# Kernel tuning notes

Hardware: AMD Instinct MI355X
Metric: run time of the kernel (lower is better)

The kernel has to match this reference:

```python
import jax, jax.numpy as jnp
from jax import lax
import numpy as np

GRID = 256   # spatial_shape of the sparse voxel volume (D=H=W)
N_ACTIVE = 500000
K = 5        # kernel_size=5, padding=2, stride=1 -> 'same' box-sum conv


def setup_inputs() -> dict:
    key = jax.random.key(0)
    k1, k2 = jax.random.split(key)
    feats = jax.random.normal(k1, (N_ACTIVE,), dtype=jnp.float32)
    coords = jax.random.randint(k2, (N_ACTIVE, 3), 0, GRID, dtype=jnp.int32)
    return {"feats": feats, "coords": coords}


def reference(feats, coords):
    # Densify the sparse tensor: scatter active-voxel features into [B=1, C=1, D, H, W].
    vol = jnp.zeros((1, 1, GRID, GRID, GRID), dtype=feats.dtype)
    vol = vol.at[0, 0, coords[:, 0], coords[:, 1], coords[:, 2]].add(feats)
    # Frozen all-ones 5x5x5 kernel (weight.data = ones, requires_grad=False), no bias.
    kernel = jnp.ones((1, 1, K, K, K), dtype=feats.dtype)  # OIDHW
    pad = K // 2
    out = lax.conv_general_dilated(
        vol, kernel,
        window_strides=(1, 1, 1),
        padding=[(pad, pad)] * 3,
        dimension_numbers=("NCDHW", "OIDHW", "NCDHW"),
    )
    # Original returns a list of one dense volume; return the array.
    return out
```

## Files before the change

kernel.cpp:

```cpp
#include <hip/hip_runtime.h>
#include <hip/hip_fp16.h>

#define GRIDN 256
#define NVOX (GRIDN * GRIDN * GRIDN)
#define NYT  32
#define NBKT (GRIDN * NYT)
#define NSUB 8
#define SBCAP 32

#define TYF   8
#define WROWS 12
#define ZS    8
#define NTHR  256

typedef float floatx4 __attribute__((ext_vector_type(4)));

#define BAR_LDS()                                              \
    do {                                                       \
        asm volatile("s_waitcnt lgkmcnt(0)" ::: "memory");     \
        __builtin_amdgcn_sched_barrier(0);                     \
        __builtin_amdgcn_s_barrier();                          \
        __builtin_amdgcn_sched_barrier(0);                     \
    } while (0)

__global__ __launch_bounds__(NTHR) void k_bin(const float* __restrict__ feats,
                                              const int* __restrict__ coords,
                                              int* __restrict__ cnt,
                                              unsigned int* __restrict__ rec, int n) {
    int i = blockIdx.x * NTHR + threadIdx.x;
    if (i >= n) return;
    int d = coords[3 * i + 0];
    int h = coords[3 * i + 1];
    int w = coords[3 * i + 2];
    int s   = blockIdx.x & (NSUB - 1);
    int key = s * NBKT + d * NYT + (h >> 3);
    int slot = atomicAdd(&cnt[key], 1);
    if (slot < SBCAP) {
        unsigned int r = (unsigned int)w | ((unsigned int)h << 8)
                       | ((unsigned int)__half_as_ushort(__float2half(feats[i])) << 16);
        rec[((size_t)key << 5) + slot] = r;
    }
}

__global__ __launch_bounds__(NTHR) void k_fused_sparse(const int* __restrict__ cnt,
                                                       const unsigned int* __restrict__ rec,
                                                       float* __restrict__ out) {
    __shared__ float Xp[3][WROWS][256];
    __shared__ int   cms[ZS + 4][24];
    __shared__ int   rbs[ZS + 4][24];

    const int tid = threadIdx.x;
    int wg  = blockIdx.x;
    int swz = (wg & 7) * 128 + (wg >> 3);
    const int y0 = (swz & 31) * TYF;
    const int z0 = (swz >> 5) * ZS;

    const int xq  = (tid & 63) * 4;
    const int yy2 = (tid >> 6) * 2;
    const int yt0 = y0 >> 3;

    for (int idx = tid; idx < (ZS + 4) * 24; idx += NTHR) {
        int k = idx / 24, q = idx - 24 * k;
        int t = q >> 3, s = q & 7;
        int zi = z0 - 2 + k;
        int yt = yt0 - 1 + t;
        int m = 0, b = 0;
        if ((unsigned)zi < (unsigned)GRIDN && (unsigned)yt < (unsigned)NYT) {
            int key = s * NBKT + zi * NYT + yt;
            m = min(cnt[key], SBCAP);
            b = key << 5;
        }
        cms[k][q] = m;
        rbs[k][q] = b;
    }
    for (int idx = tid; idx < 3 * WROWS * 64; idx += NTHR)
        ((float4*)Xp)[idx] = make_float4(0.f, 0.f, 0.f, 0.f);
    BAR_LDS();

    const int q0s = (0 * 256 + tid) >> 5, sl0 = tid & 31;
    const int q1s = (1 * 256 + tid) >> 5, sl1 = tid & 31;
    const int q2s = (2 * 256 + tid) >> 5, sl2 = tid & 31;

    auto fetch = [&](int k, unsigned int& r0, unsigned int& r1, unsigned int& r2) {
        r0 = (sl0 < cms[k][q0s]) ? rec[rbs[k][q0s] + sl0] : 0u;
        r1 = (sl1 < cms[k][q1s]) ? rec[rbs[k][q1s] + sl1] : 0u;
        r2 = (sl2 < cms[k][q2s]) ? rec[rbs[k][q2s] + sl2] : 0u;
    };

    unsigned int p0, p1, p2;
    fetch(0, p0, p1, p2);

    float4 a0 = {0,0,0,0}, a1 = {0,0,0,0}, a2 = {0,0,0,0}, a3 = {0,0,0,0}, a4 = {0,0,0,0};
    float4 b0 = {0,0,0,0}, b1 = {0,0,0,0}, b2 = {0,0,0,0}, b3 = {0,0,0,0}, b4 = {0,0,0,0};

    for (int k = 0; k <= ZS + 4; ++k) {
        unsigned int n0 = 0, n1 = 0, n2 = 0;
        if (k + 1 <= ZS + 3) fetch(k + 1, n0, n1, n2);

        if (k <= ZS + 3) {
            float (*buf)[256] = Xp[k % 3];
            auto scat = [&](unsigned int r, int ok) {
                if (!ok) return;
                int x  = r & 255;
                int y  = (r >> 8) & 255;
                int ry = y - y0 + 2;
                if ((unsigned)ry < (unsigned)WROWS) {
                    float f = __half2float(__ushort_as_half((unsigned short)(r >> 16)));
                    #pragma unroll
                    for (int dx = -2; dx <= 2; ++dx) {
                        int cc = x + dx;
                        if ((unsigned)cc < 256u)
                            atomicAdd(&buf[ry][cc], f);
                    }
                }
            };
            scat(p0, sl0 < cms[k][q0s]);
            scat(p1, sl1 < cms[k][q1s]);
            scat(p2, sl2 < cms[k][q2s]);
        }
        if (k + 1 <= ZS + 3) {
            float4* zb = (float4*)Xp[(k + 1) % 3];
            for (int idx = tid; idx < WROWS * 64; idx += NTHR)
                zb[idx] = make_float4(0.f, 0.f, 0.f, 0.f);
        }
        if (k >= 1) {
            float (*pb)[256] = Xp[(k - 1) % 3];
            float4 r0 = *(const float4*)&pb[yy2 + 0][xq];
            float4 r1 = *(const float4*)&pb[yy2 + 1][xq];
            float4 r2 = *(const float4*)&pb[yy2 + 2][xq];
            float4 r3 = *(const float4*)&pb[yy2 + 3][xq];
            float4 r4 = *(const float4*)&pb[yy2 + 4][xq];
            float4 r5 = *(const float4*)&pb[yy2 + 5][xq];
            float4 sm, v0, v1;
            sm.x = r1.x + r2.x + r3.x + r4.x;  sm.y = r1.y + r2.y + r3.y + r4.y;
            sm.z = r1.z + r2.z + r3.z + r4.z;  sm.w = r1.w + r2.w + r3.w + r4.w;
            v0.x = sm.x + r0.x; v0.y = sm.y + r0.y; v0.z = sm.z + r0.z; v0.w = sm.w + r0.w;
            v1.x = sm.x + r5.x; v1.y = sm.y + r5.y; v1.z = sm.z + r5.z; v1.w = sm.w + r5.w;
            a0 = a1; a1 = a2; a2 = a3; a3 = a4; a4 = v0;
            b0 = b1; b1 = b2; b2 = b3; b3 = b4; b4 = v1;
            int j = k - 1;
            if (j >= 4) {
                int zo = z0 + j - 4;
                floatx4 s0, s1;
                s0.x = a0.x + a1.x + a2.x + a3.x + a4.x;
                s0.y = a0.y + a1.y + a2.y + a3.y + a4.y;
                s0.z = a0.z + a1.z + a2.z + a3.z + a4.z;
                s0.w = a0.w + a1.w + a2.w + a3.w + a4.w;
                s1.x = b0.x + b1.x + b2.x + b3.x + b4.x;
                s1.y = b0.y + b1.y + b2.y + b3.y + b4.y;
                s1.z = b0.z + b1.z + b2.z + b3.z + b4.z;
                s1.w = b0.w + b1.w + b2.w + b3.w + b4.w;
                float* base = out + (size_t)zo * (GRIDN * GRIDN);
                __builtin_nontemporal_store(s0, (floatx4*)(base + (size_t)(y0 + yy2) * GRIDN + xq));
                __builtin_nontemporal_store(s1, (floatx4*)(base + (size_t)(y0 + yy2 + 1) * GRIDN + xq));
            }
        }
        BAR_LDS();
        p0 = n0; p1 = n1; p2 = n2;
    }
}

__global__ __launch_bounds__(256) void k_zero4(floatx4* __restrict__ p, int n4) {
    int stride = gridDim.x * blockDim.x;
    floatx4 z = {0.f, 0.f, 0.f, 0.f};
    for (int i = blockIdx.x * blockDim.x + threadIdx.x; i < n4; i += stride)
        __builtin_nontemporal_store(z, &p[i]);
}

__global__ void k_scatter125(const float* __restrict__ feats,
                             const int* __restrict__ coords,
                             float* __restrict__ out, int n) {
    int i = blockIdx.x * blockDim.x + threadIdx.x;
    if (i >= n) return;
    int d = coords[3 * i + 0];
    int h = coords[3 * i + 1];
    int w = coords[3 * i + 2];
    float f = feats[i];
    int d0 = max(d - 2, 0), d1 = min(d + 2, GRIDN - 1);
    int h0 = max(h - 2, 0), h1 = min(h + 2, GRIDN - 1);
    int w0 = max(w - 2, 0), w1 = min(w + 2, GRIDN - 1);
    for (int dd = d0; dd <= d1; ++dd)
        for (int hh = h0; hh <= h1; ++hh)
            for (int ww = w0; ww <= w1; ++ww)
                atomicAdd(&out[(dd * GRIDN + hh) * GRIDN + ww], f);
}

extern "C" void kernel_launch(void* const* d_in, const int* in_sizes, int n_in,
                              void* d_out, int out_size, void* d_ws, size_t ws_size,
                              hipStream_t stream) {
    const float* feats  = (const float*)d_in[0];
    const int*   coords = (const int*)d_in[1];
    float*       out    = (float*)d_out;
    int n = in_sizes[0];

    const size_t cnt_bytes = (size_t)NSUB * NBKT * sizeof(int);
    const size_t rec_bytes = (size_t)NSUB * NBKT * SBCAP * sizeof(unsigned int);

    if (ws_size >= cnt_bytes + rec_bytes) {
        int*          cnt = (int*)d_ws;
        unsigned int* rec = (unsigned int*)((char*)d_ws + cnt_bytes);
        hipMemsetAsync(cnt, 0, cnt_bytes, stream);
        k_bin<<<(n + NTHR - 1) / NTHR, NTHR, 0, stream>>>(feats, coords, cnt, rec, n);
        k_fused_sparse<<<1024, NTHR, 0, stream>>>(cnt, rec, out);
    } else {
        k_zero4<<<4096, 256, 0, stream>>>((floatx4*)out, NVOX / 4);
        k_scatter125<<<(n + 255) / 256, 256, 0, stream>>>(feats, coords, out, n);
    }
}
```

Measured before the change: 75.78 us.

## Halve z-slab per block and switch to double-buffered LDS planes

Reduces each workgroup's z-slab from 8 to 4 output planes, which doubles the grid to 2048 blocks. The LDS plane ring shrinks from three buffers to two, lowering shared memory per block so more blocks can be resident. The loop now puts two barriers in each iteration: one before scattering into the current buffer and one before the y/z reduction reads it. The cost is a larger share of halo work, since 8 slices are scattered for every 4 outputs instead of 12 for 8, plus the extra barrier per slice.

```diff
diff --git a/kernel.cpp b/kernel.cpp
--- a/kernel.cpp
+++ b/kernel.cpp
@@ -10,7 +10,8 @@
 
 #define TYF   8
 #define WROWS 12
-#define ZS    8
+#define ZS    4
+#define NITER (ZS + 4)
 #define NTHR  256
 
 typedef float floatx4 __attribute__((ext_vector_type(4)));
@@ -45,13 +46,13 @@
 __global__ __launch_bounds__(NTHR) void k_fused_sparse(const int* __restrict__ cnt,
                                                        const unsigned int* __restrict__ rec,
                                                        float* __restrict__ out) {
-    __shared__ float Xp[3][WROWS][256];
-    __shared__ int   cms[ZS + 4][24];
-    __shared__ int   rbs[ZS + 4][24];
+    __shared__ float Xp[2][WROWS][256];
+    __shared__ int   cms[NITER][24];
+    __shared__ int   rbs[NITER][24];
 
     const int tid = threadIdx.x;
     int wg  = blockIdx.x;
-    int swz = (wg & 7) * 128 + (wg >> 3);
+    int swz = (wg & 7) * 256 + (wg >> 3);
     const int y0 = (swz & 31) * TYF;
     const int z0 = (swz >> 5) * ZS;
 
@@ -59,7 +60,7 @@
     const int yy2 = (tid >> 6) * 2;
     const int yt0 = y0 >> 3;
 
-    for (int idx = tid; idx < (ZS + 4) * 24; idx += NTHR) {
+    for (int idx = tid; idx < NITER * 24; idx += NTHR) {
         int k = idx / 24, q = idx - 24 * k;
         int t = q >> 3, s = q & 7;
         int zi = z0 - 2 + k;
@@ -73,18 +74,18 @@
         cms[k][q] = m;
         rbs[k][q] = b;
     }
-    for (int idx = tid; idx < 3 * WROWS * 64; idx += NTHR)
+    for (int idx = tid; idx < 2 * WROWS * 64; idx += NTHR)
         ((float4*)Xp)[idx] = make_float4(0.f, 0.f, 0.f, 0.f);
     BAR_LDS();
 
-    const int q0s = (0 * 256 + tid) >> 5, sl0 = tid & 31;
-    const int q1s = (1 * 256 + tid) >> 5, sl1 = tid & 31;
-    const int q2s = (2 * 256 + tid) >> 5, sl2 = tid & 31;
+    const int q0s = (0 * 256 + tid) >> 5, sl = tid & 31;
+    const int q1s = (1 * 256 + tid) >> 5;
+    const int q2s = (2 * 256 + tid) >> 5;
 
     auto fetch = [&](int k, unsigned int& r0, unsigned int& r1, unsigned int& r2) {
-        r0 = (sl0 < cms[k][q0s]) ? rec[rbs[k][q0s] + sl0] : 0u;
-        r1 = (sl1 < cms[k][q1s]) ? rec[rbs[k][q1s] + sl1] : 0u;
-        r2 = (sl2 < cms[k][q2s]) ? rec[rbs[k][q2s] + sl2] : 0u;
+        r0 = (sl < cms[k][q0s]) ? rec[rbs[k][q0s] + sl] : 0u;
+        r1 = (sl < cms[k][q1s]) ? rec[rbs[k][q1s] + sl] : 0u;
+        r2 = (sl < cms[k][q2s]) ? rec[rbs[k][q2s] + sl] : 0u;
     };
 
     unsigned int p0, p1, p2;
@@ -93,12 +94,13 @@
     float4 a0 = {0,0,0,0}, a1 = {0,0,0,0}, a2 = {0,0,0,0}, a3 = {0,0,0,0}, a4 = {0,0,0,0};
     float4 b0 = {0,0,0,0}, b1 = {0,0,0,0}, b2 = {0,0,0,0}, b3 = {0,0,0,0}, b4 = {0,0,0,0};
 
-    for (int k = 0; k <= ZS + 4; ++k) {
+    for (int k = 0; k < NITER; ++k) {
+        const int cbuf = k & 1;
+        BAR_LDS();
         unsigned int n0 = 0, n1 = 0, n2 = 0;
-        if (k + 1 <= ZS + 3) fetch(k + 1, n0, n1, n2);
-
-        if (k <= ZS + 3) {
-            float (*buf)[256] = Xp[k % 3];
+        if (k + 1 < NITER) fetch(k + 1, n0, n1, n2);
+        {
+            float (*buf)[256] = Xp[cbuf];
             auto scat = [&](unsigned int r, int ok) {
                 if (!ok) return;
                 int x  = r & 255;
@@ -114,17 +116,13 @@
                     }
                 }
             };
-            scat(p0, sl0 < cms[k][q0s]);
-            scat(p1, sl1 < cms[k][q1s]);
-            scat(p2, sl2 < cms[k][q2s]);
-        }
-        if (k + 1 <= ZS + 3) {
-            float4* zb = (float4*)Xp[(k + 1) % 3];
-            for (int idx = tid; idx < WROWS * 64; idx += NTHR)
-                zb[idx] = make_float4(0.f, 0.f, 0.f, 0.f);
-        }
-        if (k >= 1) {
-            float (*pb)[256] = Xp[(k - 1) % 3];
+            scat(p0, sl < cms[k][q0s]);
+            scat(p1, sl < cms[k][q1s]);
+            scat(p2, sl < cms[k][q2s]);
+        }
+        BAR_LDS();
+        {
+            float (*pb)[256] = Xp[cbuf];
             float4 r0 = *(const float4*)&pb[yy2 + 0][xq];
             float4 r1 = *(const float4*)&pb[yy2 + 1][xq];
             float4 r2 = *(const float4*)&pb[yy2 + 2][xq];
@@ -138,24 +136,27 @@
             v1.x = sm.x + r5.x; v1.y = sm.y + r5.y; v1.z = sm.z + r5.z; v1.w = sm.w + r5.w;
             a0 = a1; a1 = a2; a2 = a3; a3 = a4; a4 = v0;
             b0 = b1; b1 = b2; b2 = b3; b3 = b4; b4 = v1;
-            int j = k - 1;
-            if (j >= 4) {
-                int zo = z0 + j - 4;
-                floatx4 s0, s1;
-                s0.x = a0.x + a1.x + a2.x + a3.x + a4.x;
-                s0.y = a0.y + a1.y + a2.y + a3.y + a4.y;
-                s0.z = a0.z + a1.z + a2.z + a3.z + a4.z;
-                s0.w = a0.w + a1.w + a2.w + a3.w + a4.w;
-                s1.x = b0.x + b1.x + b2.x + b3.x + b4.x;
-                s1.y = b0.y + b1.y + b2.y + b3.y + b4.y;
-                s1.z = b0.z + b1.z + b2.z + b3.z + b4.z;
-                s1.w = b0.w + b1.w + b2.w + b3.w + b4.w;
-                float* base = out + (size_t)zo * (GRIDN * GRIDN);
-                __builtin_nontemporal_store(s0, (floatx4*)(base + (size_t)(y0 + yy2) * GRIDN + xq));
-                __builtin_nontemporal_store(s1, (floatx4*)(base + (size_t)(y0 + yy2 + 1) * GRIDN + xq));
-            }
-        }
-        BAR_LDS();
+        }
+        if (k + 1 < NITER) {
+            float4* zb = (float4*)Xp[cbuf ^ 1];
+            for (int idx = tid; idx < WROWS * 64; idx += NTHR)
+                zb[idx] = make_float4(0.f, 0.f, 0.f, 0.f);
+        }
+        if (k >= 4) {
+            int zo = z0 + k - 4;
+            floatx4 s0, s1;
+            s0.x = a0.x + a1.x + a2.x + a3.x + a4.x;
+            s0.y = a0.y + a1.y + a2.y + a3.y + a4.y;
+            s0.z = a0.z + a1.z + a2.z + a3.z + a4.z;
+            s0.w = a0.w + a1.w + a2.w + a3.w + a4.w;
+            s1.x = b0.x + b1.x + b2.x + b3.x + b4.x;
+            s1.y = b0.y + b1.y + b2.y + b3.y + b4.y;
+            s1.z = b0.z + b1.z + b2.z + b3.z + b4.z;
+            s1.w = b0.w + b1.w + b2.w + b3.w + b4.w;
+            float* base = out + (size_t)zo * (GRIDN * GRIDN);
+            __builtin_nontemporal_store(s0, (floatx4*)(base + (size_t)(y0 + yy2) * GRIDN + xq));
+            __builtin_nontemporal_store(s1, (floatx4*)(base + (size_t)(y0 + yy2 + 1) * GRIDN + xq));
+        }
         p0 = n0; p1 = n1; p2 = n2;
     }
 }
@@ -201,7 +202,7 @@
         unsigned int* rec = (unsigned int*)((char*)d_ws + cnt_bytes);
         hipMemsetAsync(cnt, 0, cnt_bytes, stream);
         k_bin<<<(n + NTHR - 1) / NTHR, NTHR, 0, stream>>>(feats, coords, cnt, rec, n);
-        k_fused_sparse<<<1024, NTHR, 0, stream>>>(cnt, rec, out);
+        k_fused_sparse<<<(GRIDN / TYF) * (GRIDN / ZS), NTHR, 0, stream>>>(cnt, rec, out);
     } else {
         k_zero4<<<4096, 256, 0, stream>>>((floatx4*)out, NVOX / 4);
         k_scatter125<<<(n + 255) / 256, 256, 0, stream>>>(feats, coords, out, n);
```

Measured after the change: 90.70 us. 19.7% more time.
